# Kernel tuning notes

Measured on AMD Instinct MI355X. Metric: run time of the kernel, lower is better.

The kernel has to match this reference:

```python
import jax, jax.numpy as jnp
import numpy as np
from jax import lax

K = 10
EPS = 1e-12

def _l2norm(v):
    # F.normalize: v / max(||v||_2, eps) along last dim
    n = jnp.sqrt(jnp.sum(v * v, axis=-1, keepdims=True))
    return v / jnp.maximum(n, EPS)

def setup_inputs() -> dict:
    key = jax.random.key(0)
    ks = jax.random.split(key, 10)
    N, F_in, H, C, E = 100000, 512, 128, 40, 1600000
    x = jax.random.normal(ks[0], (N, F_in), dtype=jnp.float32)
    edge_index = jax.random.randint(ks[1], (2, E), 0, N, dtype=jnp.int64)
    s1 = 1.0 / np.sqrt(F_in)
    W1 = jax.random.uniform(ks[2], (F_in, H), jnp.float32, -s1, s1)
    b1 = jax.random.uniform(ks[3], (H,), jnp.float32, -s1, s1)
    s2 = 1.0 / np.sqrt(H)
    proj_w = jax.random.uniform(ks[4], (H, 1), jnp.float32, -s2, s2)
    proj_b = jax.random.uniform(ks[5], (1,), jnp.float32, -s2, s2)
    hop_w = jax.random.normal(ks[6], (1, K + 1), dtype=jnp.float32) * 0.1  # glorot-ish
    W2 = jax.random.uniform(ks[7], (H, C), jnp.float32, -s2, s2)
    b2 = jax.random.uniform(ks[8], (C,), jnp.float32, -s2, s2)
    return {"x": x, "edge_index": edge_index, "W1": W1, "b1": b1,
            "proj_w": proj_w, "proj_b": proj_b, "hop_w": hop_w,
            "W2": W2, "b2": b2}

def reference(x, edge_index, W1, b1, proj_w, proj_b, hop_w, W2, b2):
    N = x.shape[0]
    # Net: dropout (eval -> identity), lin1 + selu
    h = jax.nn.selu(x @ W1 + b1)  # [N, H]

    # --- gcn_norm with added self-loops ---
    loops = jnp.arange(N, dtype=edge_index.dtype)
    row = jnp.concatenate([edge_index[0], loops])
    col = jnp.concatenate([edge_index[1], loops])
    ew = jnp.ones(row.shape[0], dtype=h.dtype)
    deg = jax.ops.segment_sum(ew, col, num_segments=N)  # [N]
    dinv = jnp.where(deg > 0, lax.rsqrt(deg), 0.0)
    norm = dinv[row] * ew * dinv[col]  # [E+N]

    # --- K hops of scatter-add propagation ---
    def hop(xc, _):
        xn = jax.ops.segment_sum(norm[:, None] * xc[row], col, num_segments=N)
        return xn, xn
    _, hops = lax.scan(hop, h, None, length=K)  # [K, N, H]
    pps = jnp.concatenate([h[None], hops], axis=0).transpose(1, 0, 2)  # [N, K+1, H]

    # attention-weighted hop pooling
    feature_pool = (pps @ proj_w + proj_b)[..., 0]      # [N, K+1]
    m = feature_pool.mean(axis=0)                        # [K+1]
    share_w = _l2norm(m + hop_w)                         # [1, K+1]
    self_w = _l2norm(feature_pool)                       # [N, K+1]
    share = jnp.einsum('k,nkh->nh', share_w[0], pps)     # [N, H]
    selfr = jnp.einsum('nk,nkh->nh', self_w, pps)        # [N, H]
    out_prop = 0.2 * share + 0.8 * selfr

    h2 = jnp.tanh(out_prop)
    logits = h2 @ W2 + b2
    return jax.nn.log_softmax(logits, axis=1)
```

## Files before the change

### kernel.cpp

```cpp
#include <hip/hip_runtime.h>

typedef unsigned int uint;
typedef unsigned short ushort;

typedef short short8 __attribute__((ext_vector_type(8)));
typedef float floatx4 __attribute__((ext_vector_type(4)));
typedef uint uintx4 __attribute__((ext_vector_type(4)));

#define FIN 512
#define HF  128
#define NC  40
#define KHOPS 10

__device__ __forceinline__ ushort f2bf(float f) {
    uint u = __float_as_uint(f);
    uint r = (u + 0x7fffu + ((u >> 16) & 1u)) >> 16;
    return (ushort)r;
}
__device__ __forceinline__ float bflo(uint v) { return __uint_as_float(v << 16); }
__device__ __forceinline__ float bfhi(uint v) { return __uint_as_float(v & 0xffff0000u); }
__device__ __forceinline__ uint packbf2(float a, float b) {
    return (uint)f2bf(a) | ((uint)f2bf(b) << 16);
}
__device__ __forceinline__ uint cvtpk(float lo, float hi) {
    uint r;
    asm("v_cvt_pk_bf16_f32 %0, %1, %2" : "=v"(r) : "v"(lo), "v"(hi));
    return r;
}
__device__ __forceinline__ float selu_f(float v) {
    const float l = 1.0507009873554805f, a = 1.6732632423543772f;
    return v > 0.f ? l * v : l * a * (expf(v) - 1.f);
}

__global__ void k_w1frag(const float* __restrict__ W1, ushort* __restrict__ w1f) {
    int id = blockIdx.x * 256 + threadIdx.x;
    if (id >= 16 * 8 * 64) return;
    int l = id & 63;
    int t = (id >> 6) & 7;
    int s = id >> 9;
    int row0 = s * 32 + (l >> 4) * 8;
    int col  = t * 16 + (l & 15);
    ushort* dst = w1f + (size_t)id * 8;
#pragma unroll
    for (int i = 0; i < 8; ++i)
        dst[i] = f2bf(W1[(row0 + i) * HF + col]);
}

__global__ void k_w2frag(const float* __restrict__ W2, ushort* __restrict__ w2f) {
    int id = blockIdx.x * 256 + threadIdx.x;
    if (id >= 12 * 64) return;
    int l = id & 63;
    int tile = id >> 6;
    int kk = tile / 3, t = tile % 3;
    int row0 = kk * 32 + (l >> 4) * 8;
    int col  = t * 16 + (l & 15);
    ushort* dst = w2f + (size_t)id * 8;
#pragma unroll
    for (int i = 0; i < 8; ++i)
        dst[i] = (col < NC) ? f2bf(W2[(row0 + i) * NC + col]) : (ushort)0;
}

__global__ __launch_bounds__(256) void k_gemm(
        const float* __restrict__ x, const ushort* __restrict__ w1f,
        const float* __restrict__ b1, ushort* __restrict__ h,
        const float* __restrict__ projw, const float* __restrict__ projb,
        float* __restrict__ fp0, int N) {
    int tid = threadIdx.x;
    int lane = tid & 63, w = tid >> 6;
    int rowblk = blockIdx.x * 128 + w * 32;
    int kq = (lane >> 4) * 8;

    int r0 = rowblk + (lane & 15);
    int r1 = r0 + 16;
    size_t r0c = (size_t)min(r0, N - 1) * FIN;
    size_t r1c = (size_t)min(r1, N - 1) * FIN;

    floatx4 acc[2][8];
#pragma unroll
    for (int rt = 0; rt < 2; ++rt)
#pragma unroll
        for (int t = 0; t < 8; ++t) acc[rt][t] = (floatx4){0.f, 0.f, 0.f, 0.f};

    float4 aC[4];
    short8 bC[8];
    {
        const float* p0 = x + r0c + kq;
        const float* p1 = x + r1c + kq;
        aC[0] = *(const float4*)p0; aC[1] = *(const float4*)(p0 + 4);
        aC[2] = *(const float4*)p1; aC[3] = *(const float4*)(p1 + 4);
        const ushort* wp = w1f + ((size_t)lane) * 8;
#pragma unroll
        for (int t = 0; t < 8; ++t) bC[t] = *(const short8*)(wp + (size_t)t * 512);
    }

#pragma unroll 1
    for (int kk = 0; kk < 16; ++kk) {
        float4 aN[4];
        short8 bN[8];
        if (kk < 15) {
            int kb = (kk + 1) * 32 + kq;
            const float* p0 = x + r0c + kb;
            const float* p1 = x + r1c + kb;
            aN[0] = *(const float4*)p0; aN[1] = *(const float4*)(p0 + 4);
            aN[2] = *(const float4*)p1; aN[3] = *(const float4*)(p1 + 4);
            const ushort* wp = w1f + ((size_t)((kk + 1) * 8) * 64 + lane) * 8;
#pragma unroll
            for (int t = 0; t < 8; ++t) bN[t] = *(const short8*)(wp + (size_t)t * 512);
        }
        uintx4 pa0, pa1;
        pa0.x = cvtpk(aC[0].x, aC[0].y); pa0.y = cvtpk(aC[0].z, aC[0].w);
        pa0.z = cvtpk(aC[1].x, aC[1].y); pa0.w = cvtpk(aC[1].z, aC[1].w);
        pa1.x = cvtpk(aC[2].x, aC[2].y); pa1.y = cvtpk(aC[2].z, aC[2].w);
        pa1.z = cvtpk(aC[3].x, aC[3].y); pa1.w = cvtpk(aC[3].z, aC[3].w);
        short8 af0 = __builtin_bit_cast(short8, pa0);
        short8 af1 = __builtin_bit_cast(short8, pa1);
#pragma unroll
        for (int t = 0; t < 8; ++t) {
            acc[0][t] = __builtin_amdgcn_mfma_f32_16x16x32_bf16(af0, bC[t], acc[0][t], 0, 0, 0);
            acc[1][t] = __builtin_amdgcn_mfma_f32_16x16x32_bf16(af1, bC[t], acc[1][t], 0, 0, 0);
        }
        if (kk < 15) {
#pragma unroll
            for (int i = 0; i < 4; ++i) aC[i] = aN[i];
#pragma unroll
            for (int t = 0; t < 8; ++t) bC[t] = bN[t];
        }
    }

    int col0 = lane & 15;
    float fpd[2][4];
#pragma unroll
    for (int rt = 0; rt < 2; ++rt)
#pragma unroll
        for (int q = 0; q < 4; ++q) fpd[rt][q] = 0.f;
#pragma unroll
    for (int t = 0; t < 8; ++t) {
        int col = t * 16 + col0;
        float bias = b1[col];
        float pw = projw[col];
#pragma unroll
        for (int rt = 0; rt < 2; ++rt) {
#pragma unroll
            for (int q = 0; q < 4; ++q) {
                int row = rowblk + rt * 16 + (lane >> 4) * 4 + q;
                float v = selu_f(acc[rt][t][q] + bias);
                if (row < N) h[(size_t)row * HF + col] = f2bf(v);
                fpd[rt][q] = fmaf(v, pw, fpd[rt][q]);
            }
        }
    }
#pragma unroll
    for (int rt = 0; rt < 2; ++rt)
#pragma unroll
        for (int q = 0; q < 4; ++q) {
            float d = fpd[rt][q];
#pragma unroll
            for (int m = 1; m < 16; m <<= 1) d += __shfl_xor(d, m);
            fpd[rt][q] = d;
        }
    if (col0 == 0) {
        float pb = projb[0];
#pragma unroll
        for (int rt = 0; rt < 2; ++rt)
#pragma unroll
            for (int q = 0; q < 4; ++q) {
                int row = rowblk + rt * 16 + (lane >> 4) * 4 + q;
                if (row < N) fp0[row] = fpd[rt][q] + pb;
            }
    }
}

__global__ void k_deg_init(int* __restrict__ deg, int N) {
    int i = blockIdx.x * 256 + threadIdx.x;
    if (i < N) deg[i] = 1;
}
__global__ void k_deg(const int* __restrict__ ei, int* __restrict__ deg, int E) {
    int e = blockIdx.x * 256 + threadIdx.x;
    if (e < E) atomicAdd(&deg[ei[E + e]], 1);
}
__global__ void k_dinv(const int* __restrict__ deg, float* __restrict__ dinv, int N) {
    int i = blockIdx.x * 256 + threadIdx.x;
    if (i < N) dinv[i] = rsqrtf((float)deg[i]);
}

__global__ void k_scan1(const int* __restrict__ deg, int* __restrict__ offs,
                        int* __restrict__ bsum, int N) {
    __shared__ int lds[256];
    int tid = threadIdx.x;
    int base = blockIdx.x * 1024;
    int c[4], s = 0;
#pragma unroll
    for (int i = 0; i < 4; ++i) {
        int g = base + tid * 4 + i;
        c[i] = (g < N) ? (deg[g] - 1) : 0;
        s += c[i];
    }
    lds[tid] = s;
    __syncthreads();
    for (int off = 1; off < 256; off <<= 1) {
        int add = (tid >= off) ? lds[tid - off] : 0;
        __syncthreads();
        lds[tid] += add;
        __syncthreads();
    }
    int run = lds[tid] - s;
#pragma unroll
    for (int i = 0; i < 4; ++i) {
        int g = base + tid * 4 + i;
        if (g < N) offs[g] = run;
        run += c[i];
    }
    if (tid == 0) bsum[blockIdx.x] = lds[255];
}
__global__ void k_scan2(int* __restrict__ bsum, int nb) {
    if (blockIdx.x == 0 && threadIdx.x == 0) {
        int run = 0;
        for (int i = 0; i < nb; ++i) { int v = bsum[i]; bsum[i] = run; run += v; }
    }
}
__global__ void k_scan3(int* __restrict__ offs, const int* __restrict__ bsum, int N, int E) {
    int g = blockIdx.x * 256 + threadIdx.x;
    if (g < N) offs[g] += bsum[g >> 10];
    else if (g == N) offs[N] = E;
}

__global__ void k_fill(const int* __restrict__ ei, const int* __restrict__ offs,
                       int* __restrict__ cursor, int2* __restrict__ edat,
                       const float* __restrict__ dinv, int E) {
    int e = blockIdx.x * 256 + threadIdx.x;
    if (e >= E) return;
    int r = ei[e], c = ei[E + e];
    int p = offs[c] + atomicAdd(&cursor[c], 1);
    edat[p] = make_int2(r, __float_as_int(dinv[r] * dinv[c]));
}

__global__ __launch_bounds__(256) void k_hop(
                      const ushort* __restrict__ xin, ushort* __restrict__ xout,
                      const int* __restrict__ offs, const int2* __restrict__ edat,
                      const float* __restrict__ dinv,
                      const float* __restrict__ projw, const float* __restrict__ projb,
                      float* __restrict__ fpk, int N) {
    int wid = (blockIdx.x * blockDim.x + threadIdx.x) >> 6;
    int lane = threadIdx.x & 63;
    if (wid >= N) return;
    const uint* xin2 = (const uint*)xin;
    float dn = dinv[wid];
    uint sv = xin2[(size_t)wid * 64 + lane];
    float wself = dn * dn;
    float acc0 = wself * bflo(sv);
    float acc1 = wself * bfhi(sv);
    int s = offs[wid], e = offs[wid + 1];
    for (int base = s; base < e; base += 64) {
        int idx = base + lane;
        int idxc = min(idx, e - 1);
        int2 ed = edat[idxc];
        int src = ed.x;
        float ew = (idx < e) ? __int_as_float(ed.y) : 0.f;
        int cnt = min(64, e - base);
        if (cnt <= 16) {
            uint xv[16];
            float wv[16];
#pragma unroll
            for (int u = 0; u < 16; ++u) {
                int sj = __builtin_amdgcn_readlane(src, u);
                wv[u] = __int_as_float(__builtin_amdgcn_readlane(__float_as_int(ew), u));
                xv[u] = xin2[(size_t)(uint)sj * 64 + lane];
            }
#pragma unroll
            for (int u = 0; u < 16; ++u) {
                acc0 = fmaf(wv[u], bflo(xv[u]), acc0);
                acc1 = fmaf(wv[u], bfhi(xv[u]), acc1);
            }
        } else {
            int groups = (cnt + 31) >> 5;
            for (int g = 0; g < groups; ++g) {
                int j = g * 32;
                uint xv[32];
                float wv[32];
#pragma unroll
                for (int u = 0; u < 32; ++u) {
                    int sj = __builtin_amdgcn_readlane(src, j + u);
                    wv[u] = __int_as_float(__builtin_amdgcn_readlane(__float_as_int(ew), j + u));
                    xv[u] = xin2[(size_t)(uint)sj * 64 + lane];
                }
#pragma unroll
                for (int u = 0; u < 32; ++u) {
                    acc0 = fmaf(wv[u], bflo(xv[u]), acc0);
                    acc1 = fmaf(wv[u], bfhi(xv[u]), acc1);
                }
            }
        }
    }
    ((uint*)xout)[(size_t)wid * 64 + lane] = packbf2(acc0, acc1);
    float dot = acc0 * projw[2 * lane] + acc1 * projw[2 * lane + 1];
#pragma unroll
    for (int m = 1; m < 64; m <<= 1) dot += __shfl_xor(dot, m);
    if (lane == 0) fpk[wid] = dot + projb[0];
}

__global__ void k_msum(const float* __restrict__ fp, float* __restrict__ msum, int N) {
    int k = blockIdx.y;
    int i = blockIdx.x * 256 + threadIdx.x;
    int tid = threadIdx.x;
    float v = (i < N) ? fp[(size_t)k * N + i] : 0.f;
#pragma unroll
    for (int m = 1; m < 64; m <<= 1) v += __shfl_xor(v, m);
    __shared__ float ws4[4];
    if ((tid & 63) == 0) ws4[tid >> 6] = v;
    __syncthreads();
    if (tid == 0) atomicAdd(&msum[k], ws4[0] + ws4[1] + ws4[2] + ws4[3]);
}

__global__ void k_sharew(const float* __restrict__ msum, const float* __restrict__ hopw,
                         float* __restrict__ sharew, int N) {
    int k = threadIdx.x;
    float s = (k < KHOPS + 1) ? (msum[k] / (float)N + hopw[k]) : 0.f;
    float ss = s * s;
#pragma unroll
    for (int m = 1; m < 64; m <<= 1) ss += __shfl_xor(ss, m);
    float inv = 1.f / fmaxf(sqrtf(ss), 1e-12f);
    if (k < KHOPS + 1) sharew[k] = s * inv;
}

__global__ __launch_bounds__(256) void k_out(
                     const ushort* __restrict__ hops, const float* __restrict__ fp,
                     const float* __restrict__ sharew, const ushort* __restrict__ w2f,
                     const float* __restrict__ b2, float* __restrict__ out, int N) {
    __shared__ __align__(16) char As[16 * 256];
    int tid = threadIdx.x;
    int nloc = tid >> 4;
    int fg = tid & 15;
    int node = blockIdx.x * 16 + nloc;
    bool valid = node < N;
    int nodec = valid ? node : N - 1;
    const uint* hops2 = (const uint*)hops;

    float c[KHOPS + 1];
    float ss = 0.f;
#pragma unroll
    for (int k = 0; k <= KHOPS; ++k) {
        float f = fp[(size_t)k * N + nodec];
        c[k] = f;
        ss += f * f;
    }
    float inv = 1.f / fmaxf(sqrtf(ss), 1e-12f);
#pragma unroll
    for (int k = 0; k <= KHOPS; ++k)
        c[k] = valid ? (0.2f * sharew[k] + 0.8f * c[k] * inv) : 0.f;

    const uint* base = hops2 + (size_t)nodec * 64 + fg * 4;
    size_t kstr = (size_t)N * 64;
    float a[8];
#pragma unroll
    for (int j = 0; j < 8; ++j) a[j] = 0.f;
#pragma unroll
    for (int k = 0; k <= KHOPS; ++k) {
        uint4 v = *(const uint4*)(base + (size_t)k * kstr);
        float ck = c[k];
        a[0] = fmaf(ck, bflo(v.x), a[0]);
        a[1] = fmaf(ck, bfhi(v.x), a[1]);
        a[2] = fmaf(ck, bflo(v.y), a[2]);
        a[3] = fmaf(ck, bfhi(v.y), a[3]);
        a[4] = fmaf(ck, bflo(v.z), a[4]);
        a[5] = fmaf(ck, bfhi(v.z), a[5]);
        a[6] = fmaf(ck, bflo(v.w), a[6]);
        a[7] = fmaf(ck, bfhi(v.w), a[7]);
    }
    uint4 pk;
    pk.x = packbf2(tanhf(a[0]), tanhf(a[1]));
    pk.y = packbf2(tanhf(a[2]), tanhf(a[3]));
    pk.z = packbf2(tanhf(a[4]), tanhf(a[5]));
    pk.w = packbf2(tanhf(a[6]), tanhf(a[7]));
    {
        int slotbyte = fg * 16;
        int addr = nloc * 256 + (slotbyte ^ ((nloc & 15) << 4));
        *(uint4*)(As + addr) = pk;
    }
    __syncthreads();

    int w = tid >> 6, lane = tid & 63;
    floatx4 acc = (floatx4){0.f, 0.f, 0.f, 0.f};
    if (w < 3) {
        int r = lane & 15;
#pragma unroll
        for (int kk = 0; kk < 4; ++kk) {
            int slotbyte = kk * 64 + (lane >> 4) * 16;
            int addr = r * 256 + (slotbyte ^ ((r & 15) << 4));
            short8 af = *(const short8*)(As + addr);
            const short8 bf = *(const short8*)(w2f + (size_t)((kk * 3 + w) * 64 + lane) * 8);
            acc = __builtin_amdgcn_mfma_f32_16x16x32_bf16(af, bf, acc, 0, 0, 0);
        }
    }
    __syncthreads();

    float* Ls = (float*)As;
    if (w < 3) {
        int cls = w * 16 + (lane & 15);
        float bb = (cls < NC) ? b2[cls] : 0.f;
#pragma unroll
        for (int q = 0; q < 4; ++q) {
            int row = (lane >> 4) * 4 + q;
            Ls[row * 48 + cls] = acc[q] + bb;
        }
    }
    __syncthreads();

    int r2 = tid >> 4;
    int c16 = tid & 15;
    float v0 = Ls[r2 * 48 + c16];
    float v1 = Ls[r2 * 48 + 16 + c16];
    bool has2 = c16 < 8;
    float v2 = has2 ? Ls[r2 * 48 + 32 + c16] : -INFINITY;
    float lm = fmaxf(fmaxf(v0, v1), v2);
#pragma unroll
    for (int m = 1; m < 16; m <<= 1) lm = fmaxf(lm, __shfl_xor(lm, m));
    float se = expf(v0 - lm) + expf(v1 - lm) + (has2 ? expf(v2 - lm) : 0.f);
#pragma unroll
    for (int m = 1; m < 16; m <<= 1) se += __shfl_xor(se, m);
    float lse = lm + logf(se);
    int nodeo = blockIdx.x * 16 + r2;
    if (nodeo < N) {
        out[(size_t)nodeo * NC + c16] = v0 - lse;
        out[(size_t)nodeo * NC + 16 + c16] = v1 - lse;
        if (has2) out[(size_t)nodeo * NC + 32 + c16] = v2 - lse;
    }
}

extern "C" void kernel_launch(void* const* d_in, const int* in_sizes, int n_in,
                              void* d_out, int out_size, void* d_ws, size_t ws_size,
                              hipStream_t stream) {
    const float* x     = (const float*)d_in[0];
    const int*   ei    = (const int*)d_in[1];
    const float* W1    = (const float*)d_in[2];
    const float* b1    = (const float*)d_in[3];
    const float* projw = (const float*)d_in[4];
    const float* projb = (const float*)d_in[5];
    const float* hopw  = (const float*)d_in[6];
    const float* W2    = (const float*)d_in[7];
    const float* b2    = (const float*)d_in[8];
    float* out = (float*)d_out;

    int N = in_sizes[0] / FIN;
    int E = in_sizes[1] / 2;

    char* p = (char*)d_ws;
    auto alloc = [&](size_t bytes) -> char* {
        char* r = p;
        p += (bytes + 255) & ~(size_t)255;
        return r;
    };
    ushort* hops   = (ushort*)alloc((size_t)(KHOPS + 1) * N * HF * 2);
    int*    deg    = (int*)alloc((size_t)N * 4);
    float*  dinv   = (float*)alloc((size_t)N * 4);
    int*    offs   = (int*)alloc((size_t)(N + 1) * 4);
    int*    cursor = (int*)alloc((size_t)N * 4);
    int*    bsum   = (int*)alloc(4096);
    int2*   edat   = (int2*)alloc((size_t)E * 8);
    float*  fp     = (float*)alloc((size_t)(KHOPS + 1) * N * 4);
    float*  msum   = (float*)alloc(64);
    float*  sharew = (float*)alloc(64);
    ushort* w1f    = (ushort*)alloc((size_t)FIN * HF * 2);
    ushort* w2f    = (ushort*)alloc((size_t)12 * 64 * 8 * 2);

    int nb256N = (N + 255) / 256;
    int nbE    = (E + 255) / 256;
    int nbWave = (N + 3) / 4;
    int nb1024 = (N + 1023) / 1024;

    k_w1frag<<<32, 256, 0, stream>>>(W1, w1f);
    k_w2frag<<<3, 256, 0, stream>>>(W2, w2f);
    k_gemm<<<(N + 127) / 128, 256, 0, stream>>>(x, w1f, b1, hops, projw, projb, fp, N);

    k_deg_init<<<nb256N, 256, 0, stream>>>(deg, N);
    k_deg<<<nbE, 256, 0, stream>>>(ei, deg, E);
    k_dinv<<<nb256N, 256, 0, stream>>>(deg, dinv, N);

    k_scan1<<<nb1024, 256, 0, stream>>>(deg, offs, bsum, N);
    k_scan2<<<1, 64, 0, stream>>>(bsum, nb1024);
    k_scan3<<<(N + 256) / 256, 256, 0, stream>>>(offs, bsum, N, E);

    hipMemsetAsync(cursor, 0, (size_t)N * 4, stream);
    k_fill<<<nbE, 256, 0, stream>>>(ei, offs, cursor, edat, dinv, E);

    for (int k = 1; k <= KHOPS; ++k) {
        const ushort* xin = hops + (size_t)(k - 1) * N * HF;
        ushort* xout      = hops + (size_t)k * N * HF;
        k_hop<<<nbWave, 256, 0, stream>>>(xin, xout, offs, edat, dinv,
                                          projw, projb, fp + (size_t)k * N, N);
    }

    hipMemsetAsync(msum, 0, 64, stream);
    dim3 gm(nb256N, KHOPS + 1);
    k_msum<<<gm, 256, 0, stream>>>(fp, msum, N);
    k_sharew<<<1, 64, 0, stream>>>(msum, hopw, sharew, N);

    k_out<<<(N + 15) / 16, 256, 0, stream>>>(hops, fp, sharew, w2f, b2, out, N);
}
```

Before: 1.029 ms.

## Stage GEMM x tiles via global_load_lds double-buffering; unify propagation gather groups

```diff
diff --git a/kernel.cpp b/kernel.cpp
--- a/kernel.cpp
+++ b/kernel.cpp
@@ -31,6 +31,11 @@
     const float l = 1.0507009873554805f, a = 1.6732632423543772f;
     return v > 0.f ? l * v : l * a * (expf(v) - 1.f);
 }
+
+#define GLDS16(g, l)                                                        \
+    __builtin_amdgcn_global_load_lds(                                       \
+        (const __attribute__((address_space(1))) void*)(g),                 \
+        (__attribute__((address_space(3))) void*)(l), 16, 0, 0)
 
 __global__ void k_w1frag(const float* __restrict__ W1, ushort* __restrict__ w1f) {
     int id = blockIdx.x * 256 + threadIdx.x;
@@ -65,15 +70,17 @@
         const float* __restrict__ b1, ushort* __restrict__ h,
         const float* __restrict__ projw, const float* __restrict__ projb,
         float* __restrict__ fp0, int N) {
+    __shared__ __align__(16) float bufA[4][32 * 32];
+    __shared__ __align__(16) float bufB[4][32 * 32];
     int tid = threadIdx.x;
     int lane = tid & 63, w = tid >> 6;
     int rowblk = blockIdx.x * 128 + w * 32;
-    int kq = (lane >> 4) * 8;
-
-    int r0 = rowblk + (lane & 15);
-    int r1 = r0 + 16;
-    size_t r0c = (size_t)min(r0, N - 1) * FIN;
-    size_t r1c = (size_t)min(r1, N - 1) * FIN;
+
+    int srl = lane >> 3;
+    int ssl = lane & 7;
+    int srcoff = ((ssl ^ srl) << 2);
+    float* bA = bufA[w];
+    float* bB = bufB[w];
 
     floatx4 acc[2][8];
 #pragma unroll
@@ -81,50 +88,65 @@
 #pragma unroll
         for (int t = 0; t < 8; ++t) acc[rt][t] = (floatx4){0.f, 0.f, 0.f, 0.f};
 
-    float4 aC[4];
-    short8 bC[8];
-    {
-        const float* p0 = x + r0c + kq;
-        const float* p1 = x + r1c + kq;
-        aC[0] = *(const float4*)p0; aC[1] = *(const float4*)(p0 + 4);
-        aC[2] = *(const float4*)p1; aC[3] = *(const float4*)(p1 + 4);
-        const ushort* wp = w1f + ((size_t)lane) * 8;
-#pragma unroll
-        for (int t = 0; t < 8; ++t) bC[t] = *(const short8*)(wp + (size_t)t * 512);
-    }
-
+    short8 bE[8], bO[8];
+
+    auto STAGE = [&](float* lbuf, int kk) {
+        int k0 = kk * 32;
+#pragma unroll
+        for (int i = 0; i < 4; ++i) {
+            int row = rowblk + i * 8 + srl;
+            const float* g = x + (size_t)min(row, N - 1) * FIN + k0 + srcoff;
+            GLDS16(g, lbuf + i * 256);
+        }
+    };
+    auto LOADB = [&](short8* bb, int kk) {
+        const ushort* wp = w1f + ((size_t)(kk * 8) * 64 + lane) * 8;
+#pragma unroll
+        for (int t = 0; t < 8; ++t) bb[t] = *(const short8*)(wp + (size_t)t * 512);
+    };
+
+    int rl16 = lane & 15, cq = lane >> 4;
+    int lo_sl = ((2 * cq) ^ (rl16 & 7)) << 4;
+    int hi_sl = ((2 * cq + 1) ^ (rl16 & 7)) << 4;
+
+    auto COMPUTE = [&](const float* lbuf, short8* bb) {
+#pragma unroll
+        for (int rt = 0; rt < 2; ++rt) {
+            const char* rbase = (const char*)lbuf + (rt * 16 + rl16) * 128;
+            float4 lo = *(const float4*)(rbase + lo_sl);
+            float4 hi = *(const float4*)(rbase + hi_sl);
+            uintx4 pa;
+            pa.x = cvtpk(lo.x, lo.y); pa.y = cvtpk(lo.z, lo.w);
+            pa.z = cvtpk(hi.x, hi.y); pa.w = cvtpk(hi.z, hi.w);
+            short8 af = __builtin_bit_cast(short8, pa);
+#pragma unroll
+            for (int t = 0; t < 8; ++t)
+                acc[rt][t] = __builtin_amdgcn_mfma_f32_16x16x32_bf16(af, bb[t], acc[rt][t], 0, 0, 0);
+        }
+    };
+
+    STAGE(bA, 0);
+    LOADB(bE, 0);
 #pragma unroll 1
-    for (int kk = 0; kk < 16; ++kk) {
-        float4 aN[4];
-        short8 bN[8];
-        if (kk < 15) {
-            int kb = (kk + 1) * 32 + kq;
-            const float* p0 = x + r0c + kb;
-            const float* p1 = x + r1c + kb;
-            aN[0] = *(const float4*)p0; aN[1] = *(const float4*)(p0 + 4);
-            aN[2] = *(const float4*)p1; aN[3] = *(const float4*)(p1 + 4);
-            const ushort* wp = w1f + ((size_t)((kk + 1) * 8) * 64 + lane) * 8;
-#pragma unroll
-            for (int t = 0; t < 8; ++t) bN[t] = *(const short8*)(wp + (size_t)t * 512);
-        }
-        uintx4 pa0, pa1;
-        pa0.x = cvtpk(aC[0].x, aC[0].y); pa0.y = cvtpk(aC[0].z, aC[0].w);
-        pa0.z = cvtpk(aC[1].x, aC[1].y); pa0.w = cvtpk(aC[1].z, aC[1].w);
-        pa1.x = cvtpk(aC[2].x, aC[2].y); pa1.y = cvtpk(aC[2].z, aC[2].w);
-        pa1.z = cvtpk(aC[3].x, aC[3].y); pa1.w = cvtpk(aC[3].z, aC[3].w);
-        short8 af0 = __builtin_bit_cast(short8, pa0);
-        short8 af1 = __builtin_bit_cast(short8, pa1);
-#pragma unroll
-        for (int t = 0; t < 8; ++t) {
-            acc[0][t] = __builtin_amdgcn_mfma_f32_16x16x32_bf16(af0, bC[t], acc[0][t], 0, 0, 0);
-            acc[1][t] = __builtin_amdgcn_mfma_f32_16x16x32_bf16(af1, bC[t], acc[1][t], 0, 0, 0);
-        }
-        if (kk < 15) {
-#pragma unroll
-            for (int i = 0; i < 4; ++i) aC[i] = aN[i];
-#pragma unroll
-            for (int t = 0; t < 8; ++t) bC[t] = bN[t];
-        }
+    for (int kk = 0; kk < 16; kk += 2) {
+        asm volatile("s_waitcnt lgkmcnt(0)" ::: "memory");
+        __builtin_amdgcn_sched_barrier(0);
+        STAGE(bB, kk + 1);
+        LOADB(bO, kk + 1);
+        asm volatile("s_waitcnt vmcnt(12)" ::: "memory");
+        __builtin_amdgcn_sched_barrier(0);
+        COMPUTE(bA, bE);
+        asm volatile("s_waitcnt lgkmcnt(0)" ::: "memory");
+        __builtin_amdgcn_sched_barrier(0);
+        if (kk + 2 < 16) {
+            STAGE(bA, kk + 2);
+            LOADB(bE, kk + 2);
+            asm volatile("s_waitcnt vmcnt(12)" ::: "memory");
+        } else {
+            asm volatile("s_waitcnt vmcnt(0)" ::: "memory");
+        }
+        __builtin_amdgcn_sched_barrier(0);
+        COMPUTE(bB, bO);
     }
 
     int col0 = lane & 15;
@@ -257,37 +279,21 @@
         int src = ed.x;
         float ew = (idx < e) ? __int_as_float(ed.y) : 0.f;
         int cnt = min(64, e - base);
-        if (cnt <= 16) {
+        int groups = (cnt + 15) >> 4;
+        for (int g = 0; g < groups; ++g) {
+            int j = g * 16;
             uint xv[16];
             float wv[16];
 #pragma unroll
             for (int u = 0; u < 16; ++u) {
-                int sj = __builtin_amdgcn_readlane(src, u);
-                wv[u] = __int_as_float(__builtin_amdgcn_readlane(__float_as_int(ew), u));
+                int sj = __builtin_amdgcn_readlane(src, j + u);
+                wv[u] = __int_as_float(__builtin_amdgcn_readlane(__float_as_int(ew), j + u));
                 xv[u] = xin2[(size_t)(uint)sj * 64 + lane];
             }
 #pragma unroll
             for (int u = 0; u < 16; ++u) {
                 acc0 = fmaf(wv[u], bflo(xv[u]), acc0);
                 acc1 = fmaf(wv[u], bfhi(xv[u]), acc1);
-            }
-        } else {
-            int groups = (cnt + 31) >> 5;
-            for (int g = 0; g < groups; ++g) {
-                int j = g * 32;
-                uint xv[32];
-                float wv[32];
-#pragma unroll
-                for (int u = 0; u < 32; ++u) {
-                    int sj = __builtin_amdgcn_readlane(src, j + u);
-                    wv[u] = __int_as_float(__builtin_amdgcn_readlane(__float_as_int(ew), j + u));
-                    xv[u] = xin2[(size_t)(uint)sj * 64 + lane];
-                }
-#pragma unroll
-                for (int u = 0; u < 32; ++u) {
-                    acc0 = fmaf(wv[u], bflo(xv[u]), acc0);
-                    acc1 = fmaf(wv[u], bfhi(xv[u]), acc1);
-                }
             }
         }
     }
```

After: 968.3 us. 5.9% less time.
